# Optimization experiments

Measured on AMD Instinct MI355X. Metric: run time of the kernel, lower is better.

The kernel has to match this reference:

```python
import jax, jax.numpy as jnp
import numpy as np

B, D, L = 16384, 1024, 4

def setup_inputs() -> dict:
    key = jax.random.key(0)
    k1, k2 = jax.random.split(key)
    inputs = jax.random.normal(k1, (B, D), dtype=jnp.float32)
    # xavier_uniform for (D, 1): bound = sqrt(6/(D+1))
    bound = float(np.sqrt(6.0 / (D + 1)))
    weights = jax.random.uniform(k2, (L, D), dtype=jnp.float32, minval=-bound, maxval=bound)
    biases = jnp.zeros((L, D), dtype=jnp.float32)
    return {"inputs": inputs, "weights": weights, "biases": biases}

def reference(inputs, weights, biases):
    # inputs: [B, D]; weights/biases: [L, D]
    x0 = inputs

    def step(x, wb):
        w, b = wb
        xw = jnp.einsum("bd,d->b", x, w)          # x^T w  -> [B]
        x_next = x0 * xw[:, None] + b[None, :] + x  # outer product + bias + residual
        return x_next, None

    out, _ = jax.lax.scan(step, x0, (weights, biases))
    return out
```

## Files before the change

### kernel.cpp

```cpp
#include <hip/hip_runtime.h>


#define NB 16384
#define NWAVES 4
#define NBLOCKS (NB / NWAVES)

#define DOT4(a, b) ((a).x*(b).x + (a).y*(b).y + (a).z*(b).z + (a).w*(b).w)

__device__ __forceinline__ float wave_sum64(float v) {
  float r = v;
  r += __int_as_float(__builtin_amdgcn_update_dpp(
      0, __float_as_int(r), 0x111, 0xf, 0xf, false));
  r += __int_as_float(__builtin_amdgcn_update_dpp(
      0, __float_as_int(r), 0x112, 0xf, 0xf, false));
  r += __int_as_float(__builtin_amdgcn_update_dpp(
      0, __float_as_int(r), 0x114, 0xf, 0xf, false));
  r += __int_as_float(__builtin_amdgcn_update_dpp(
      0, __float_as_int(r), 0x118, 0xf, 0xf, false));
  r += __int_as_float(__builtin_amdgcn_update_dpp(
      0, __float_as_int(r), 0x142, 0xa, 0xf, false));
  r += __int_as_float(__builtin_amdgcn_update_dpp(
      0, __float_as_int(r), 0x143, 0xc, 0xf, false));
  return r;
}

__device__ __forceinline__ float bcast63(float v) {
  return __int_as_float(__builtin_amdgcn_readlane(__float_as_int(v), 63));
}

__global__ __launch_bounds__(256, 4) void crossnet_fused(
    const float* __restrict__ X,
    const float* __restrict__ W,
    const float* __restrict__ Bias,
    float* __restrict__ Out) {
  __shared__ float4 lds_u4[256];
  __shared__ float lds_s[NWAVES][3];

  const int t = threadIdx.x;
  const int wave = t >> 6;
  const int lane = t & 63;
  const int row = blockIdx.x * NWAVES + wave;

  const float4* W4 = (const float4*)W;
  const float4* B4 = (const float4*)Bias;
  const float4* Xr = (const float4*)X + (size_t)row * 256;
  float4* Or = (float4*)Out + (size_t)row * 256;

  float4 x[4];
#pragma unroll
  for (int k = 0; k < 4; ++k) x[k] = Xr[lane + 64 * k];

  float4 w[4][4];
#pragma unroll
  for (int l = 0; l < 4; ++l)
#pragma unroll
    for (int k = 0; k < 4; ++k)
      w[l][k] = W4[l * 256 + lane + 64 * k];

  float4 b0 = B4[t];
  float4 b1 = B4[256 + t];
  float4 b2 = B4[512 + t];
  float4 b3 = B4[768 + t];
  float4 w1t = W4[256 + t];
  float4 w2t = W4[512 + t];
  float4 w3t = W4[768 + t];

  float4 u = b0;
  float s1p = DOT4(u, w1t);
  u.x += b1.x; u.y += b1.y; u.z += b1.z; u.w += b1.w;
  float s2p = DOT4(u, w2t);
  u.x += b2.x; u.y += b2.y; u.z += b2.z; u.w += b2.w;
  float s3p = DOT4(u, w3t);
  u.x += b3.x; u.y += b3.y; u.z += b3.z; u.w += b3.w;
  lds_u4[t] = u;

  s1p = wave_sum64(s1p);
  s2p = wave_sum64(s2p);
  s3p = wave_sum64(s3p);
  if (lane == 63) {
    lds_s[wave][0] = s1p;
    lds_s[wave][1] = s2p;
    lds_s[wave][2] = s3p;
  }

  float p0 = 0.f, p1 = 0.f, p2 = 0.f, p3 = 0.f;
#pragma unroll
  for (int k = 0; k < 4; ++k) {
    p0 += DOT4(x[k], w[0][k]);
    p1 += DOT4(x[k], w[1][k]);
    p2 += DOT4(x[k], w[2][k]);
    p3 += DOT4(x[k], w[3][k]);
  }
  const float P0 = bcast63(wave_sum64(p0));
  const float P1 = bcast63(wave_sum64(p1));
  const float P2 = bcast63(wave_sum64(p2));
  const float P3 = bcast63(wave_sum64(p3));

  __syncthreads();

  const float s1 = lds_s[0][0] + lds_s[1][0] + lds_s[2][0] + lds_s[3][0];
  const float s2 = lds_s[0][1] + lds_s[1][1] + lds_s[2][1] + lds_s[3][1];
  const float s3 = lds_s[0][2] + lds_s[1][2] + lds_s[2][2] + lds_s[3][2];

  float c = P0 + 1.0f;
  c = c * (P1 + 1.0f) + s1;
  c = c * (P2 + 1.0f) + s2;
  c = c * (P3 + 1.0f) + s3;

#pragma unroll
  for (int k = 0; k < 4; ++k) {
    float4 u4r = lds_u4[lane + 64 * k];
    float4 o;
    o.x = c * x[k].x + u4r.x;
    o.y = c * x[k].y + u4r.y;
    o.z = c * x[k].z + u4r.z;
    o.w = c * x[k].w + u4r.w;
    Or[lane + 64 * k] = o;
  }
}

extern "C" void kernel_launch(void* const* d_in, const int* in_sizes, int n_in,
                              void* d_out, int out_size, void* d_ws, size_t ws_size,
                              hipStream_t stream) {
  const float* X = (const float*)d_in[0];
  const float* W = (const float*)d_in[1];
  const float* Bias = (const float*)d_in[2];
  float* Out = (float*)d_out;

  crossnet_fused<<<NBLOCKS, 256, 0, stream>>>(X, W, Bias, Out);
}
```

Before: 26.91 us.

## Split bias-only scalars into prologue kernel and process two rows per wave

Moves the bias-only terms (cumulative bias vector u and the scalars s1..s3) into a tiny single-wave kernel that writes them to workspace. The main kernel then drops its LDS staging and __syncthreads and handles two rows per wave so each weight load is reused. X loads and output stores become nontemporal. This removes redundant per-block bias work and the barrier, at the cost of an extra kernel launch and a serial dependency between the two kernels.

Measured after the change: 50.03 us. 86.0% more time.

```diff
diff --git a/kernel.cpp b/kernel.cpp
--- a/kernel.cpp
+++ b/kernel.cpp
@@ -2,8 +2,10 @@
 
 
 #define NB 16384
-#define NWAVES 4
-#define NBLOCKS (NB / NWAVES)
+#define ROWS_PER_WAVE 2
+#define NBLOCKS (NB / (4 * ROWS_PER_WAVE))
+
+typedef float f32x4 __attribute__((ext_vector_type(4)));
 
 #define DOT4(a, b) ((a).x*(b).x + (a).y*(b).y + (a).z*(b).z + (a).w*(b).w)
 
@@ -28,94 +30,115 @@
   return __int_as_float(__builtin_amdgcn_readlane(__float_as_int(v), 63));
 }
 
-__global__ __launch_bounds__(256, 4) void crossnet_fused(
-    const float* __restrict__ X,
+__global__ __launch_bounds__(64) void crossnet_scalars(
     const float* __restrict__ W,
     const float* __restrict__ Bias,
-    float* __restrict__ Out) {
-  __shared__ float4 lds_u4[256];
-  __shared__ float lds_s[NWAVES][3];
+    float* __restrict__ ws) {
+  const int lane = threadIdx.x;
+  const f32x4* W4 = (const f32x4*)W;
+  const f32x4* B4 = (const f32x4*)Bias;
 
-  const int t = threadIdx.x;
-  const int wave = t >> 6;
-  const int lane = t & 63;
-  const int row = blockIdx.x * NWAVES + wave;
-
-  const float4* W4 = (const float4*)W;
-  const float4* B4 = (const float4*)Bias;
-  const float4* Xr = (const float4*)X + (size_t)row * 256;
-  float4* Or = (float4*)Out + (size_t)row * 256;
-
-  float4 x[4];
+  float s1p = 0.f, s2p = 0.f, s3p = 0.f;
+  f32x4 u[4];
 #pragma unroll
-  for (int k = 0; k < 4; ++k) x[k] = Xr[lane + 64 * k];
-
-  float4 w[4][4];
-#pragma unroll
-  for (int l = 0; l < 4; ++l)
-#pragma unroll
-    for (int k = 0; k < 4; ++k)
-      w[l][k] = W4[l * 256 + lane + 64 * k];
-
-  float4 b0 = B4[t];
-  float4 b1 = B4[256 + t];
-  float4 b2 = B4[512 + t];
-  float4 b3 = B4[768 + t];
-  float4 w1t = W4[256 + t];
-  float4 w2t = W4[512 + t];
-  float4 w3t = W4[768 + t];
-
-  float4 u = b0;
-  float s1p = DOT4(u, w1t);
-  u.x += b1.x; u.y += b1.y; u.z += b1.z; u.w += b1.w;
-  float s2p = DOT4(u, w2t);
-  u.x += b2.x; u.y += b2.y; u.z += b2.z; u.w += b2.w;
-  float s3p = DOT4(u, w3t);
-  u.x += b3.x; u.y += b3.y; u.z += b3.z; u.w += b3.w;
-  lds_u4[t] = u;
-
+  for (int k = 0; k < 4; ++k) {
+    const int idx = lane + 64 * k;
+    f32x4 b0 = B4[idx];
+    f32x4 b1 = B4[256 + idx];
+    f32x4 b2 = B4[512 + idx];
+    f32x4 b3 = B4[768 + idx];
+    f32x4 w1 = W4[256 + idx];
+    f32x4 w2 = W4[512 + idx];
+    f32x4 w3 = W4[768 + idx];
+    f32x4 uu = b0;
+    s1p += DOT4(uu, w1);
+    uu += b1;
+    s2p += DOT4(uu, w2);
+    uu += b2;
+    s3p += DOT4(uu, w3);
+    uu += b3;
+    u[k] = uu;
+  }
   s1p = wave_sum64(s1p);
   s2p = wave_sum64(s2p);
   s3p = wave_sum64(s3p);
   if (lane == 63) {
-    lds_s[wave][0] = s1p;
-    lds_s[wave][1] = s2p;
-    lds_s[wave][2] = s3p;
+    ws[0] = 0.0f;
+    ws[1] = s1p;
+    ws[2] = s2p;
+    ws[3] = s3p;
+  }
+  f32x4* U4 = (f32x4*)(ws + 4);
+#pragma unroll
+  for (int k = 0; k < 4; ++k) U4[lane + 64 * k] = u[k];
+}
+
+__global__ __launch_bounds__(256, 5) void crossnet_main(
+    const float* __restrict__ X,
+    const float* __restrict__ W,
+    const float* __restrict__ ws,
+    float* __restrict__ Out) {
+  const int wave = threadIdx.x >> 6;
+  const int lane = threadIdx.x & 63;
+  const int row0 = (blockIdx.x * 4 + wave) * ROWS_PER_WAVE;
+
+  const f32x4* Xa = (const f32x4*)X + (size_t)row0 * 256;
+  const f32x4* Xb = Xa + 256;
+  f32x4* Oa = (f32x4*)Out + (size_t)row0 * 256;
+  f32x4* Ob = Oa + 256;
+  const f32x4* W4 = (const f32x4*)W;
+
+  f32x4 xa[4], xb[4];
+#pragma unroll
+  for (int k = 0; k < 4; ++k) xa[k] = __builtin_nontemporal_load(&Xa[lane + 64 * k]);
+#pragma unroll
+  for (int k = 0; k < 4; ++k) xb[k] = __builtin_nontemporal_load(&Xb[lane + 64 * k]);
+
+  float pa0 = 0.f, pa1 = 0.f, pa2 = 0.f, pa3 = 0.f;
+  float pb0 = 0.f, pb1 = 0.f, pb2 = 0.f, pb3 = 0.f;
+#pragma unroll
+  for (int l = 0; l < 4; ++l) {
+    f32x4 w0 = W4[l * 256 + lane];
+    f32x4 w1 = W4[l * 256 + lane + 64];
+    f32x4 w2 = W4[l * 256 + lane + 128];
+    f32x4 w3 = W4[l * 256 + lane + 192];
+    float da = DOT4(xa[0], w0) + DOT4(xa[1], w1) + DOT4(xa[2], w2) + DOT4(xa[3], w3);
+    float db = DOT4(xb[0], w0) + DOT4(xb[1], w1) + DOT4(xb[2], w2) + DOT4(xb[3], w3);
+    if (l == 0) { pa0 = da; pb0 = db; }
+    else if (l == 1) { pa1 = da; pb1 = db; }
+    else if (l == 2) { pa2 = da; pb2 = db; }
+    else { pa3 = da; pb3 = db; }
   }
 
-  float p0 = 0.f, p1 = 0.f, p2 = 0.f, p3 = 0.f;
+  const f32x4* U4 = (const f32x4*)(ws + 4);
+  f32x4 u4r[4];
 #pragma unroll
-  for (int k = 0; k < 4; ++k) {
-    p0 += DOT4(x[k], w[0][k]);
-    p1 += DOT4(x[k], w[1][k]);
-    p2 += DOT4(x[k], w[2][k]);
-    p3 += DOT4(x[k], w[3][k]);
-  }
-  const float P0 = bcast63(wave_sum64(p0));
-  const float P1 = bcast63(wave_sum64(p1));
-  const float P2 = bcast63(wave_sum64(p2));
-  const float P3 = bcast63(wave_sum64(p3));
+  for (int k = 0; k < 4; ++k) u4r[k] = U4[lane + 64 * k];
+  const f32x4 sv = *(const f32x4*)ws;
 
-  __syncthreads();
+  pa0 = wave_sum64(pa0); pa1 = wave_sum64(pa1);
+  pa2 = wave_sum64(pa2); pa3 = wave_sum64(pa3);
+  pb0 = wave_sum64(pb0); pb1 = wave_sum64(pb1);
+  pb2 = wave_sum64(pb2); pb3 = wave_sum64(pb3);
 
-  const float s1 = lds_s[0][0] + lds_s[1][0] + lds_s[2][0] + lds_s[3][0];
-  const float s2 = lds_s[0][1] + lds_s[1][1] + lds_s[2][1] + lds_s[3][1];
-  const float s3 = lds_s[0][2] + lds_s[1][2] + lds_s[2][2] + lds_s[3][2];
-
-  float c = P0 + 1.0f;
-  c = c * (P1 + 1.0f) + s1;
-  c = c * (P2 + 1.0f) + s2;
-  c = c * (P3 + 1.0f) + s3;
+  float ca = bcast63(pa0) + 1.0f;
+  ca = ca * (bcast63(pa1) + 1.0f) + sv.y;
+  ca = ca * (bcast63(pa2) + 1.0f) + sv.z;
+  ca = ca * (bcast63(pa3) + 1.0f) + sv.w;
+  float cb = bcast63(pb0) + 1.0f;
+  cb = cb * (bcast63(pb1) + 1.0f) + sv.y;
+  cb = cb * (bcast63(pb2) + 1.0f) + sv.z;
+  cb = cb * (bcast63(pb3) + 1.0f) + sv.w;
 
 #pragma unroll
   for (int k = 0; k < 4; ++k) {
-    float4 u4r = lds_u4[lane + 64 * k];
-    float4 o;
-    o.x = c * x[k].x + u4r.x;
-    o.y = c * x[k].y + u4r.y;
-    o.z = c * x[k].z + u4r.z;
-    o.w = c * x[k].w + u4r.w;
-    Or[lane + 64 * k] = o;
+    f32x4 o = ca * xa[k] + u4r[k];
+    __builtin_nontemporal_store(o, &Oa[lane + 64 * k]);
+  }
+#pragma unroll
+  for (int k = 0; k < 4; ++k) {
+    f32x4 o = cb * xb[k] + u4r[k];
+    __builtin_nontemporal_store(o, &Ob[lane + 64 * k]);
   }
 }
 
@@ -126,6 +149,8 @@
   const float* W = (const float*)d_in[1];
   const float* Bias = (const float*)d_in[2];
   float* Out = (float*)d_out;
+  float* ws = (float*)d_ws;
 
-  crossnet_fused<<<NBLOCKS, 256, 0, stream>>>(X, W, Bias, Out);
+  crossnet_scalars<<<1, 64, 0, stream>>>(W, Bias, ws);
+  crossnet_main<<<NBLOCKS, 256, 0, stream>>>(X, W, ws, Out);
 }
```
